# Performance work log

Hardware: AMD Instinct MI355X
Metric: run time of the kernel (lower is better)

The kernel has to match this reference:

```python
import jax, jax.numpy as jnp
import numpy as np

B, S, D_MODEL = 2, 1024, 1024
N_HEADS, D_QK, D_V = 16, 64, 64
MAX_ROPE, MAX_REL = 2048, 128
ATTN_SCALE = 8.0  # sqrt(d_qk)
BASE = 10000.0


def _rope_table():
    # sinusoidal buffer from RoPE.__init__ (pos_type='sinusoidal')
    pos = np.arange(MAX_ROPE).reshape(-1, 1)
    ang = pos / np.power(BASE, np.arange(0, D_QK, 2).reshape(1, -1) / D_QK)
    W = np.zeros((MAX_ROPE, D_QK), dtype=np.float32)
    W[:, 0::2] = np.sin(ang)
    W[:, 1::2] = np.cos(ang)
    return jnp.asarray(W)


def _apply_rope(x, pe):
    # x: [b,n,s,d], pe: [b,s,d]
    cos = jnp.tile(pe[:, :, 1::2], (1, 1, 2))[:, None, :, :]  # [b,1,s,d]
    sin = jnp.tile(pe[:, :, 0::2], (1, 1, 2))[:, None, :, :]
    half = D_QK // 2
    x2 = jnp.concatenate([-x[..., half:], x[..., :half]], axis=-1)
    return x * cos + x2 * sin


def setup_inputs() -> dict:
    key = jax.random.key(0)
    ks = jax.random.split(key, 12)
    w_scale = 1.0 / np.sqrt(D_MODEL)
    inp = {
        'query': jax.random.normal(ks[0], (B, S, D_MODEL), jnp.float32),
        'key': jax.random.normal(ks[1], (B, S, D_MODEL), jnp.float32),
        'value': jax.random.normal(ks[2], (B, S, D_MODEL), jnp.float32),
        'attn_mask': jnp.broadcast_to(jnp.triu(jnp.ones((S, S), bool), 1), (B, S, S)),
        'q_pos_ids': jnp.broadcast_to(jnp.arange(S, dtype=jnp.int32), (B, S)),
        'kv_pos_ids': jnp.broadcast_to(jnp.arange(S, dtype=jnp.int32), (B, S)),
        'W_q': jax.random.normal(ks[3], (N_HEADS * D_QK, D_MODEL), jnp.float32) * w_scale,
        'b_q': jnp.zeros((N_HEADS * D_QK,), jnp.float32),
        'W_k': jax.random.normal(ks[4], (N_HEADS * D_QK, D_MODEL), jnp.float32) * w_scale,
        'b_k': jnp.zeros((N_HEADS * D_QK,), jnp.float32),
        'W_v': jax.random.normal(ks[5], (N_HEADS * D_V, D_MODEL), jnp.float32) * w_scale,
        'b_v': jnp.zeros((N_HEADS * D_V,), jnp.float32),
        'W_o': jax.random.normal(ks[6], (D_MODEL, N_HEADS * D_V), jnp.float32) * w_scale,
        'b_o': jnp.zeros((D_MODEL,), jnp.float32),
        'rel_k_table': jax.random.normal(ks[7], (2 * MAX_REL + 1, D_QK), jnp.float32) * 0.02,
        'rel_v_table': jax.random.normal(ks[8], (2 * MAX_REL + 1, D_V), jnp.float32) * 0.02,
        'w_pre': jax.random.normal(ks[9], (N_HEADS, N_HEADS), jnp.float32) * (1.0 / np.sqrt(N_HEADS)),
        'w_post': jax.random.normal(ks[10], (N_HEADS, N_HEADS), jnp.float32) * (1.0 / np.sqrt(N_HEADS)),
    }
    return inp


def reference(query, key, value, attn_mask, q_pos_ids, kv_pos_ids,
              W_q, b_q, W_k, b_k, W_v, b_v, W_o, b_o,
              rel_k_table, rel_v_table, w_pre, w_post):
    # projections: F.linear(x, W) = x @ W.T, then + bias
    q = (query @ W_q.T + b_q).reshape(B, S, N_HEADS, D_QK).transpose(0, 2, 1, 3)
    k = (key @ W_k.T + b_k).reshape(B, S, N_HEADS, D_QK).transpose(0, 2, 1, 3)
    v = (value @ W_v.T + b_v).reshape(B, S, N_HEADS, D_V).transpose(0, 2, 1, 3)

    # RoPE (sinusoidal buffer, no grad)
    rope_W = _rope_table()
    q = _apply_rope(q, rope_W[q_pos_ids])
    k = _apply_rope(k, rope_W[kv_pos_ids])

    # relative position embeddings (learned tables)
    rel_dis = q_pos_ids[:, :, None] - kv_pos_ids[:, None, :]        # [b,q,k]
    idx = jnp.clip(rel_dis, -MAX_REL, MAX_REL) + MAX_REL
    pos_key = rel_k_table[idx]                                       # [b,q,k,d_qk]
    pos_value = rel_v_table[idx]                                     # [b,q,k,d_v]

    scores = jnp.einsum('bnqd,bnkd->bnqk', q, k)
    scores = scores + jnp.einsum('bnqd,bqkd->bnqk', q, pos_key)
    scores = scores / ATTN_SCALE
    scores = jnp.einsum('bnqk,nm->bmqk', scores, w_pre)              # talking heads pre-softmax
    scores = jnp.where(attn_mask[:, None, :, :], -10000.0, scores)
    attn = jax.nn.softmax(scores, axis=-1)
    attn = jnp.einsum('bmqk,mn->bnqk', attn, w_post)                 # talking heads post-softmax

    out = jnp.einsum('bnqk,bnkd->bnqd', attn, v)
    out = out + jnp.einsum('bnqk,bqkd->bnqd', attn, pos_value)

    out = out.transpose(0, 2, 1, 3).reshape(B, S, N_HEADS * D_V)
    out = out @ W_o.T + b_o
    return out
```

## Files before the change

kernel.cpp:

```cpp
#include <hip/hip_runtime.h>

#define SEQ 1024

typedef short v8s __attribute__((ext_vector_type(8)));
typedef float v4f __attribute__((ext_vector_type(4)));

__device__ __forceinline__ short f2bfs(float f){
  unsigned int u = __float_as_uint(f);
  u += 0x7fffu + ((u >> 16) & 1u);
  return (short)(u >> 16);
}
__device__ __forceinline__ float bfl(short s){
  return __uint_as_float(((unsigned int)(unsigned short)s) << 16);
}

__global__ __launch_bounds__(256) void conv_kernel(
    const float* __restrict__ q, const float* __restrict__ k, const float* __restrict__ v,
    const float* __restrict__ wq, const float* __restrict__ wk2, const float* __restrict__ wv2,
    const float* __restrict__ wo, unsigned short* __restrict__ dst)
{
  size_t e0 = ((size_t)blockIdx.x * 256 + threadIdx.x) * 8;
  const float* src; size_t off;
  if      (e0 <  2097152){ src = q;   off = e0; }
  else if (e0 <  4194304){ src = k;   off = e0 - 2097152; }
  else if (e0 <  6291456){ src = v;   off = e0 - 4194304; }
  else if (e0 <  7340032){ src = wq;  off = e0 - 6291456; }
  else if (e0 <  8388608){ src = wk2; off = e0 - 7340032; }
  else if (e0 <  9437184){ src = wv2; off = e0 - 8388608; }
  else                   { src = wo;  off = e0 - 9437184; }
  float4 a = *(const float4*)(src + off);
  float4 b = *(const float4*)(src + off + 4);
  v8s o = { f2bfs(a.x), f2bfs(a.y), f2bfs(a.z), f2bfs(a.w),
            f2bfs(b.x), f2bfs(b.y), f2bfs(b.z), f2bfs(b.w) };
  *(v8s*)(dst + e0) = o;
}

__device__ __forceinline__ void gemm_body(
    const unsigned short* __restrict__ A16,
    const unsigned short* __restrict__ P1, const unsigned short* __restrict__ P2,
    const unsigned short* __restrict__ P3,
    const unsigned short* __restrict__ W16,
    const float* __restrict__ bias, void* __restrict__ outv,
    const int* __restrict__ pos_ids, int mode)
{
  __shared__ short As[2][64][40];
  __shared__ short Ws[2][128][40];

  int t = threadIdx.x;
  int lane = t & 63, wave = t >> 6;
  int l15 = lane & 15, quad = lane >> 4;
  int wm = wave >> 1, wn = wave & 1;
  int row0 = blockIdx.y << 6;
  int col0 = blockIdx.x << 7;

  v4f acc[4];
  #pragma unroll
  for (int j = 0; j < 4; j++) acc[j] = (v4f){0.f, 0.f, 0.f, 0.f};

  int ar = t >> 2, ac = (t & 3) * 8;
  int wr = t >> 2, wc = (t & 3) * 8;
  size_t abase = (size_t)(row0 + ar)*1024 + ac;
  size_t wbase = (size_t)(col0 + wr)*1024 + wc;

  if (t < 256){
    if (P1){
      v8s x0 = *(const v8s*)(A16 + abase);
      v8s x1 = *(const v8s*)(P1 + abase);
      v8s x2 = *(const v8s*)(P2 + abase);
      v8s x3 = *(const v8s*)(P3 + abase);
      v8s o;
      #pragma unroll
      for (int jj = 0; jj < 8; jj++)
        o[jj] = f2bfs(bfl(x0[jj]) + bfl(x1[jj]) + bfl(x2[jj]) + bfl(x3[jj]));
      *(v8s*)&As[0][ar][ac] = o;
    } else {
      *(v8s*)&As[0][ar][ac] = *(const v8s*)(A16 + abase);
    }
  }
  *(v8s*)&Ws[0][wr][wc] = *(const v8s*)(W16 + wbase);
  __syncthreads();

  int cur = 0;
  for (int kt = 0; kt < 1024; kt += 32){
    bool nxt = (kt + 32) < 1024;
    v8s a_st, x1s, x2s, x3s, w_st;
    if (nxt){
      if (t < 256){
        a_st = *(const v8s*)(A16 + abase + kt + 32);
        if (P1){
          x1s = *(const v8s*)(P1 + abase + kt + 32);
          x2s = *(const v8s*)(P2 + abase + kt + 32);
          x3s = *(const v8s*)(P3 + abase + kt + 32);
        }
      }
      w_st = *(const v8s*)(W16 + wbase + kt + 32);
    }

    v8s af = *(v8s*)&As[cur][wm*16 + l15][quad*8];
    v8s bfq[4];
    #pragma unroll
    for (int j = 0; j < 4; j++) bfq[j] = *(v8s*)&Ws[cur][wn*64 + j*16 + l15][quad*8];
    #pragma unroll
    for (int j = 0; j < 4; j++)
      acc[j] = __builtin_amdgcn_mfma_f32_16x16x32_bf16(af, bfq[j], acc[j], 0, 0, 0);

    if (nxt){
      if (t < 256){
        if (P1){
          v8s o;
          #pragma unroll
          for (int jj = 0; jj < 8; jj++)
            o[jj] = f2bfs(bfl(a_st[jj]) + bfl(x1s[jj]) + bfl(x2s[jj]) + bfl(x3s[jj]));
          *(v8s*)&As[cur ^ 1][ar][ac] = o;
        } else {
          *(v8s*)&As[cur ^ 1][ar][ac] = a_st;
        }
      }
      *(v8s*)&Ws[cur ^ 1][wr][wc] = w_st;
      __syncthreads();
      cur ^= 1;
    }
  }

  int rbase = row0 + wm*16 + quad*4;
  if (mode == 1){
    unsigned short* o16 = (unsigned short*)outv;
    int pos[4];
    #pragma unroll
    for (int r = 0; r < 4; r++){
      int p = pos_ids[rbase + r];
      pos[r] = p < 0 ? 0 : (p > 2047 ? 2047 : p);
    }
    float fr0 = exp2f(-0.4152410118609203f * (float)l15);
    float fr1 = exp2f(-0.4152410118609203f * (float)(16 + l15));
    float csv[2][4], snv[2][4];
    #pragma unroll
    for (int r = 0; r < 4; r++){
      float a0 = (float)pos[r] * fr0;
      float a1 = (float)pos[r] * fr1;
      csv[0][r] = __cosf(a0); snv[0][r] = __sinf(a0);
      csv[1][r] = __cosf(a1); snv[1][r] = __sinf(a1);
    }
    #pragma unroll
    for (int j = 0; j < 4; j++){
      int gcol = col0 + wn*64 + j*16 + l15;
      float bs = bias[gcol];
      float bp = bias[gcol ^ 32];
      #pragma unroll
      for (int r = 0; r < 4; r++){
        float x = acc[j][r] + bs;
        float p = acc[j ^ 2][r] + bp;
        float cs = csv[j & 1][r];
        float sn = snv[j & 1][r];
        float o = (j < 2) ? (x*cs - p*sn) : (x*cs + p*sn);
        o16[(size_t)(rbase + r)*1024 + gcol] = (unsigned short)f2bfs(o);
      }
    }
  } else if (mode == 2){
    unsigned short* o16 = (unsigned short*)outv;
    int bb = rbase >> 10, s0 = rbase & 1023;
    #pragma unroll
    for (int j = 0; j < 4; j++){
      int gcol = col0 + wn*64 + j*16 + l15;
      float bs = bias[gcol];
      unsigned int w0 = ((unsigned int)(unsigned short)f2bfs(acc[j][0] + bs)) |
                        (((unsigned int)(unsigned short)f2bfs(acc[j][1] + bs)) << 16);
      unsigned int w1 = ((unsigned int)(unsigned short)f2bfs(acc[j][2] + bs)) |
                        (((unsigned int)(unsigned short)f2bfs(acc[j][3] + bs)) << 16);
      uint2 pk; pk.x = w0; pk.y = w1;
      *(uint2*)&o16[((size_t)(bb*1024 + gcol))*1024 + s0] = pk;
    }
  } else {
    float* o32 = (float*)outv;
    #pragma unroll
    for (int j = 0; j < 4; j++){
      int gcol = col0 + wn*64 + j*16 + l15;
      float bs = bias[gcol];
      #pragma unroll
      for (int r = 0; r < 4; r++)
        o32[(size_t)(rbase + r)*1024 + gcol] = acc[j][r] + bs;
    }
  }
}

__global__ __launch_bounds__(512) void gemm_qkv_kernel(
    const unsigned short* __restrict__ qa, const unsigned short* __restrict__ ka,
    const unsigned short* __restrict__ va,
    const unsigned short* __restrict__ wq, const unsigned short* __restrict__ wk,
    const unsigned short* __restrict__ wv,
    const float* __restrict__ bq, const float* __restrict__ bk, const float* __restrict__ bv,
    unsigned short* __restrict__ oq, unsigned short* __restrict__ ok, unsigned short* __restrict__ ov,
    const int* __restrict__ qpos, const int* __restrict__ kpos)
{
  int z = blockIdx.z;
  const unsigned short* A16 = (z == 0) ? qa : (z == 1) ? ka : va;
  const unsigned short* W16 = (z == 0) ? wq : (z == 1) ? wk : wv;
  const float* bias         = (z == 0) ? bq : (z == 1) ? bk : bv;
  unsigned short* outp      = (z == 0) ? oq : (z == 1) ? ok : ov;
  const int* pos            = (z == 1) ? kpos : qpos;
  int mode                  = (z == 2) ? 2 : 1;
  gemm_body(A16, nullptr, nullptr, nullptr, W16, bias, (void*)outp, pos, mode);
}

__global__ __launch_bounds__(512) void gemm_o_kernel(
    const unsigned short* __restrict__ c0, const unsigned short* __restrict__ c1,
    const unsigned short* __restrict__ c2, const unsigned short* __restrict__ c3,
    const unsigned short* __restrict__ wo, const float* __restrict__ bo,
    float* __restrict__ outp)
{
  gemm_body(c0, c1, c2, c3, wo, bo, (void*)outp, nullptr, 0);
}

__global__ __launch_bounds__(1024) void attn_pass1(
    const unsigned short* __restrict__ qw, const unsigned short* __restrict__ kw,
    const float* __restrict__ relk, const float* __restrict__ wpre_g,
    unsigned short* __restrict__ Sp, float* __restrict__ Lp)
{
  __shared__ short U_t[2][512][20];
  __shared__ short W_l[16][16][48];
  __shared__ short relk_s[129][68];

  int t = threadIdx.x;
  int h = t >> 6, lane = t & 63;
  int l15 = lane & 15, quad = lane >> 4;
  int bid = blockIdx.x;
  int quarter = bid & 3;
  int b = (bid >> 2) & 1;
  int qt = 63 - (bid >> 3);
  int q0 = qt << 4;
  int nkt = (qt + 2) >> 1;
  int hq = qt >> 1;
  int offt = hq*(hq+1) + ((qt & 1) ? (hq + 1) : 0);
  unsigned short* Sbase = Sp + ((size_t)(b*1056 + offt)) * 8192;

  for (int e = t; e < 129*64; e += 1024)
    relk_s[e >> 6][e & 63] = f2bfs(relk[(size_t)(128 + (e >> 6))*64 + (e & 63)]);

  v8s awp;
  #pragma unroll
  for (int jj = 0; jj < 8; jj++){
    int n = quad*8 + jj;
    awp[jj] = (n < 16) ? f2bfs(wpre_g[n*16 + l15]) : (short)0;
  }
  v8s aq[2];
  {
    const unsigned short* qb = qw + ((size_t)(b*SEQ + q0 + l15))*1024 + h*64;
    #pragma unroll
    for (int c = 0; c < 2; c++) aq[c] = *(const v8s*)(qb + c*32 + quad*8);
  }
  __syncthreads();

  v4f cinf = (v4f){0.f,0.f,0.f,0.f};
  #pragma unroll
  for (int c = 0; c < 2; c++){
    v8s binf = *(v8s*)&relk_s[128][c*32 + quad*8];
    cinf = __builtin_amdgcn_mfma_f32_16x16x32_bf16(aq[c], binf, cinf, 0, 0, 0);
  }

  float l_part[4] = {0.f, 0.f, 0.f, 0.f};

  v8s kc[2][2];
  if (quarter < nkt){
    int k0 = quarter << 5;
    #pragma unroll
    for (int ct = 0; ct < 2; ct++){
      const unsigned short* kb = kw + ((size_t)(b*SEQ + k0 + ct*16 + l15))*1024 + h*64;
      #pragma unroll
      for (int c = 0; c < 2; c++) kc[ct][c] = *(const v8s*)(kb + c*32 + quad*8);
    }
  }

  int buf = 0;
  for (int ci = quarter; ci < nkt; ci += 4){
    int k0 = ci << 5;
    int r_lo = q0 - k0 - 31;
    bool far = (r_lo >= 128);

    v4f cqk[2];
    #pragma unroll
    for (int ct = 0; ct < 2; ct++){
      v4f acc = (v4f){0.f,0.f,0.f,0.f};
      #pragma unroll
      for (int c = 0; c < 2; c++)
        acc = __builtin_amdgcn_mfma_f32_16x16x32_bf16(aq[c], kc[ct][c], acc, 0, 0, 0);
      cqk[ct] = acc;
    }
    {
      int cin = ci + 4;
      int k0n = ((cin < nkt) ? cin : ci) << 5;
      #pragma unroll
      for (int ct = 0; ct < 2; ct++){
        const unsigned short* kb = kw + ((size_t)(b*SEQ + k0n + ct*16 + l15))*1024 + h*64;
        #pragma unroll
        for (int c = 0; c < 2; c++) kc[ct][c] = *(const v8s*)(kb + c*32 + quad*8);
      }
    }

    if (!far){
      #pragma unroll
      for (int pt = 0; pt < 3; pt++){
        int rr = r_lo + pt*16 + l15; rr = rr < 0 ? 0 : (rr > 128 ? 128 : rr);
        v4f acc = (v4f){0.f,0.f,0.f,0.f};
        #pragma unroll
        for (int c = 0; c < 2; c++){
          v8s rv = *(v8s*)&relk_s[rr][c*32 + quad*8];
          acc = __builtin_amdgcn_mfma_f32_16x16x32_bf16(aq[c], rv, acc, 0, 0, 0);
        }
        #pragma unroll
        for (int reg = 0; reg < 4; reg++)
          W_l[h][quad*4 + reg][pt*16 + l15] = f2bfs(acc[reg]);
      }
    }
    #pragma unroll
    for (int ct = 0; ct < 2; ct++)
      #pragma unroll
      for (int reg = 0; reg < 4; reg++){
        int i = quad*4 + reg, j = ct*16 + l15;
        float wv = far ? cinf[reg] : bfl(W_l[h][i][i - j + 31]);
        U_t[buf][i*32 + j][h] = f2bfs((cqk[ct][reg] + wv) * 0.125f);
      }
    __syncthreads();

    v4f cs[2];
    #pragma unroll
    for (int ct = 0; ct < 2; ct++){
      v8s bu = (v8s){0,0,0,0,0,0,0,0};
      if (quad < 2) bu = *(v8s*)&U_t[buf][h*32 + ct*16 + l15][quad*8];
      cs[ct] = __builtin_amdgcn_mfma_f32_16x16x32_bf16(awp, bu, (v4f){0.f,0.f,0.f,0.f}, 0, 0, 0);
    }
    unsigned short* stile = Sbase + (size_t)ci * 8192;
    #pragma unroll
    for (int ct = 0; ct < 2; ct++){
      bool vv = (k0 + ct*16 + l15) <= (q0 + h);
      short pb16[4];
      #pragma unroll
      for (int reg = 0; reg < 4; reg++){
        float p = vv ? __expf(cs[ct][reg]) : 0.f;
        l_part[reg] += p;
        pb16[reg] = f2bfs(p);
      }
      uint2 pk;
      pk.x = ((unsigned int)(unsigned short)pb16[0]) | (((unsigned int)(unsigned short)pb16[1]) << 16);
      pk.y = ((unsigned int)(unsigned short)pb16[2]) | (((unsigned int)(unsigned short)pb16[3]) << 16);
      *(uint2*)(stile + ((size_t)((h*2 + ct)*64 + quad*16 + l15))*4) = pk;
    }
    buf ^= 1;
  }

  #pragma unroll
  for (int reg = 0; reg < 4; reg++){
    float sm = l_part[reg];
    sm += __shfl_xor(sm, 1, 64);
    sm += __shfl_xor(sm, 2, 64);
    sm += __shfl_xor(sm, 4, 64);
    sm += __shfl_xor(sm, 8, 64);
    l_part[reg] = sm;
  }
  size_t pb = ((((size_t)b*64 + qt)*4 + quarter)*16 + h)*16;
  if (l15 == 0){
    #pragma unroll
    for (int reg = 0; reg < 4; reg++)
      Lp[pb + quad*4 + reg] = l_part[reg];
  }
}

__global__ __launch_bounds__(1024) void attn_pass2(
    const unsigned short* __restrict__ Sp, const unsigned short* __restrict__ vwT,
    const float* __restrict__ relv, const float* __restrict__ wpost_g,
    const float* __restrict__ Lp,
    unsigned short* __restrict__ c0, unsigned short* __restrict__ c1,
    unsigned short* __restrict__ c2, unsigned short* __restrict__ c3)
{
  __shared__ short U_t[512][20];
  __shared__ short Pp[2][16][16][40];
  __shared__ short relv_s[129][66];
  __shared__ float il_f[16][17], Srow[16][17];

  int t = threadIdx.x;
  int h = t >> 6, lane = t & 63;
  int l15 = lane & 15, quad = lane >> 4;
  int bid = blockIdx.x;
  int quarter = bid & 3;
  int b = (bid >> 2) & 1;
  int qt = 63 - (bid >> 3);
  int q0 = qt << 4;
  int nkt = (qt + 2) >> 1;
  int hq = qt >> 1;
  int offt = hq*(hq+1) + ((qt & 1) ? (hq + 1) : 0);
  const unsigned short* Sbase = Sp + ((size_t)(b*1056 + offt)) * 8192;
  unsigned short* ctx = (quarter == 0) ? c0 : (quarter == 1) ? c1 : (quarter == 2) ? c2 : c3;

  for (int e = t; e < 129*64; e += 1024)
    relv_s[e >> 6][e & 63] = f2bfs(relv[(size_t)(128 + (e >> 6))*64 + (e & 63)]);
  if (t < 256){
    int i = t >> 4, n = t & 15;
    size_t b0 = ((((size_t)b*64 + qt)*4 + 0)*16 + i)*16 + n;
    float l = 0.f;
    #pragma unroll
    for (int qd = 0; qd < 4; qd++) l += Lp[b0 + qd*256];
    il_f[i][n] = 1.f / l;
  }
  v8s awq;
  #pragma unroll
  for (int jj = 0; jj < 8; jj++){
    int n = quad*8 + jj;
    awq[jj] = (n < 16) ? f2bfs(wpost_g[n*16 + l15]) : (short)0;
  }
  __syncthreads();

  v4f o_acc[4];
  #pragma unroll
  for (int dt = 0; dt < 4; dt++) o_acc[dt] = (v4f){0.f,0.f,0.f,0.f};
  float sr_part[4] = {0.f, 0.f, 0.f, 0.f};

  const unsigned short* vtb = vwT + ((size_t)(b*1024 + h*64))*1024;

  uint4 sv;
  v8s bvc[4];
  if (quarter < nkt){
    sv = *(const uint4*)(Sbase + (size_t)quarter*8192 + (size_t)t*8);
    int k0 = quarter << 5;
    #pragma unroll
    for (int dt = 0; dt < 4; dt++)
      bvc[dt] = *(const v8s*)(vtb + (size_t)(dt*16 + l15)*1024 + k0 + quad*8);
  }

  int pbuf = 0;
  for (int ci = quarter; ci < nkt; ci += 4){
    int k0 = ci << 5;
    int r_lo = q0 - k0 - 31;
    bool far = (r_lo >= 128);

    #pragma unroll
    for (int g = 0; g < 2; g++){
      unsigned int w0 = (g == 0) ? sv.x : sv.z;
      unsigned int w1 = (g == 0) ? sv.y : sv.w;
      int v = t*2 + g;
      int i = v >> 7, ct = (v >> 6) & 1, quadv = (v >> 4) & 3, lv = v & 15;
      int j = ct*16 + lv;
      short at[4];
      unsigned short ss[4] = { (unsigned short)(w0 & 0xffff), (unsigned short)(w0 >> 16),
                               (unsigned short)(w1 & 0xffff), (unsigned short)(w1 >> 16) };
      #pragma unroll
      for (int reg = 0; reg < 4; reg++){
        int n = quadv*4 + reg;
        at[reg] = f2bfs(bfl((short)ss[reg]) * il_f[i][n]);
      }
      unsigned int lo = ((unsigned int)(unsigned short)at[0]) | (((unsigned int)(unsigned short)at[1]) << 16);
      unsigned int hi = ((unsigned int)(unsigned short)at[2]) | (((unsigned int)(unsigned short)at[3]) << 16);
      uint2 pk; pk.x = lo; pk.y = hi;
      *(uint2*)&U_t[i*32 + j][quadv*4] = pk;
    }

    v4f cp[2];
    #pragma unroll
    for (int ct = 0; ct < 2; ct++){
      v8s bu = (v8s){0,0,0,0,0,0,0,0};
      if (quad < 2) bu = *(v8s*)&U_t[h*32 + ct*16 + l15][quad*8];
      cp[ct] = __builtin_amdgcn_mfma_f32_16x16x32_bf16(awq, bu, (v4f){0.f,0.f,0.f,0.f}, 0, 0, 0);
    }
    #pragma unroll
    for (int ct = 0; ct < 2; ct++)
      #pragma unroll
      for (int reg = 0; reg < 4; reg++){
        int n = quad*4 + reg, j = ct*16 + l15;
        Pp[pbuf][n][h][j] = f2bfs(cp[ct][reg]);
      }
    if (far){
      #pragma unroll
      for (int reg = 0; reg < 4; reg++)
        sr_part[reg] += cp[0][reg] + cp[1][reg];
    }
    __syncthreads();

    {
      int cin = ci + 4;
      int cld = (cin < nkt) ? cin : ci;
      sv = *(const uint4*)(Sbase + (size_t)cld*8192 + (size_t)t*8);
    }

    v8s ap = *(v8s*)&Pp[pbuf][h][l15][quad*8];
    #pragma unroll
    for (int dt = 0; dt < 4; dt++)
      o_acc[dt] = __builtin_amdgcn_mfma_f32_16x16x32_bf16(ap, bvc[dt], o_acc[dt], 0, 0, 0);
    {
      int cin = ci + 4;
      int k0n = ((cin < nkt) ? cin : ci) << 5;
      #pragma unroll
      for (int dt = 0; dt < 4; dt++)
        bvc[dt] = *(const v8s*)(vtb + (size_t)(dt*16 + l15)*1024 + k0n + quad*8);
    }
    if (!far){
      #pragma unroll
      for (int ch = 0; ch < 2; ch++){
        v8s at2;
        #pragma unroll
        for (int jj = 0; jj < 8; jj++){
          int jx = l15 + 31 - (ch*32 + quad*8 + jj);
          at2[jj] = ((unsigned)jx < 32u) ? Pp[pbuf][h][l15][jx] : (short)0;
        }
        #pragma unroll
        for (int dt = 0; dt < 4; dt++){
          v8s br;
          #pragma unroll
          for (int jj = 0; jj < 8; jj++){
            int rr = r_lo + ch*32 + quad*8 + jj;
            rr = rr < 0 ? 0 : (rr > 128 ? 128 : rr);
            br[jj] = relv_s[rr][dt*16 + l15];
          }
          o_acc[dt] = __builtin_amdgcn_mfma_f32_16x16x32_bf16(at2, br, o_acc[dt], 0, 0, 0);
        }
      }
    }
    pbuf ^= 1;
  }

  #pragma unroll
  for (int reg = 0; reg < 4; reg++){
    float s = sr_part[reg];
    s += __shfl_xor(s, 1, 64);
    s += __shfl_xor(s, 2, 64);
    s += __shfl_xor(s, 4, 64);
    s += __shfl_xor(s, 8, 64);
    if (l15 == 0) Srow[quad*4 + reg][h] = s;
  }
  __syncthreads();

  #pragma unroll
  for (int dt = 0; dt < 4; dt++)
    #pragma unroll
    for (int reg = 0; reg < 4; reg++){
      float o = o_acc[dt][reg] + Srow[h][quad*4 + reg] * bfl(relv_s[128][dt*16 + l15]);
      ctx[((size_t)(b*SEQ + q0 + quad*4 + reg))*1024 + h*64 + dt*16 + l15] = (unsigned short)f2bfs(o);
    }
}

extern "C" void kernel_launch(void* const* d_in, const int* in_sizes, int n_in,
                              void* d_out, int out_size, void* d_ws, size_t ws_size,
                              hipStream_t stream)
{
  int ip = -1;
  for (int i = 0; i < n_in; i++){
    if (in_sizes[i] == 2048){ ip = i; break; }
  }
  if (ip < 0) ip = 4;

  const float* query = (const float*)d_in[0];
  const float* key   = (const float*)d_in[1];
  const float* value = (const float*)d_in[2];
  const int* qpos = (const int*)d_in[ip];
  const int* kpos = (const int*)d_in[ip + 1];
  const float* Wq    = (const float*)d_in[ip + 2];
  const float* bq    = (const float*)d_in[ip + 3];
  const float* Wk    = (const float*)d_in[ip + 4];
  const float* bk    = (const float*)d_in[ip + 5];
  const float* Wv    = (const float*)d_in[ip + 6];
  const float* b_v   = (const float*)d_in[ip + 7];
  const float* Wo    = (const float*)d_in[ip + 8];
  const float* bo    = (const float*)d_in[ip + 9];
  const float* relk  = (const float*)d_in[ip + 10];
  const float* relv  = (const float*)d_in[ip + 11];
  const float* wpre  = (const float*)d_in[ip + 12];
  const float* wpost = (const float*)d_in[ip + 13];

  char* ws = (char*)d_ws;
  unsigned short* conv  = (unsigned short*)(ws + 524288);
  unsigned short* qbf   = conv;
  unsigned short* kbf   = conv + 2097152;
  unsigned short* vbf   = conv + 4194304;
  unsigned short* wqbf  = conv + 6291456;
  unsigned short* wkbf  = conv + 7340032;
  unsigned short* wvbf  = conv + 8388608;
  unsigned short* wobf  = conv + 9437184;
  unsigned short* q_ws  = (unsigned short*)(ws + 21495808);
  unsigned short* k_ws  = (unsigned short*)(ws + 25690112);
  unsigned short* v_ws  = (unsigned short*)(ws + 29884416);
  unsigned short* ctx0  = (unsigned short*)(ws + 34078720);
  unsigned short* ctx1  = (unsigned short*)(ws + 38273024);
  unsigned short* ctx2  = (unsigned short*)(ws + 42467328);
  unsigned short* ctx3  = (unsigned short*)(ws + 46661632);
  unsigned short* Sp    = (unsigned short*)(ws + 50855936);
  float* Lp             = (float*)(ws + 85983232);

  hipLaunchKernelGGL(conv_kernel, dim3(5120), dim3(256), 0, stream,
                     query, key, value, Wq, Wk, Wv, Wo, conv);
  hipLaunchKernelGGL(gemm_qkv_kernel, dim3(8, 32, 3), dim3(512), 0, stream,
                     qbf, kbf, vbf, wqbf, wkbf, wvbf, bq, bk, b_v,
                     q_ws, k_ws, v_ws, qpos, kpos);
  hipLaunchKernelGGL(attn_pass1, dim3(512), dim3(1024), 0, stream,
                     q_ws, k_ws, relk, wpre, Sp, Lp);
  hipLaunchKernelGGL(attn_pass2, dim3(512), dim3(1024), 0, stream,
                     Sp, v_ws, relv, wpost, Lp, ctx0, ctx1, ctx2, ctx3);
  hipLaunchKernelGGL(gemm_o_kernel, dim3(8, 32), dim3(512), 0, stream,
                     ctx0, ctx1, ctx2, ctx3, wobf, bo, (float*)d_out);
}
```

Measured before the change: 248.9 us.

## Store score tiles in MFMA operand layout and fold 1/l into post weights

Result: no change. 249.9 us (+0.4%).

```diff
diff --git a/kernel.cpp b/kernel.cpp
--- a/kernel.cpp
+++ b/kernel.cpp
@@ -342,7 +342,7 @@
       uint2 pk;
       pk.x = ((unsigned int)(unsigned short)pb16[0]) | (((unsigned int)(unsigned short)pb16[1]) << 16);
       pk.y = ((unsigned int)(unsigned short)pb16[2]) | (((unsigned int)(unsigned short)pb16[3]) << 16);
-      *(uint2*)(stile + ((size_t)((h*2 + ct)*64 + quad*16 + l15))*4) = pk;
+      *(uint2*)(stile + (size_t)(h*32 + ct*16 + l15)*16 + quad*4) = pk;
     }
     buf ^= 1;
   }
@@ -371,7 +371,6 @@
     unsigned short* __restrict__ c0, unsigned short* __restrict__ c1,
     unsigned short* __restrict__ c2, unsigned short* __restrict__ c3)
 {
-  __shared__ short U_t[512][20];
   __shared__ short Pp[2][16][16][40];
   __shared__ short relv_s[129][66];
   __shared__ float il_f[16][17], Srow[16][17];
@@ -400,13 +399,16 @@
     for (int qd = 0; qd < 4; qd++) l += Lp[b0 + qd*256];
     il_f[i][n] = 1.f / l;
   }
-  v8s awq;
-  #pragma unroll
-  for (int jj = 0; jj < 8; jj++){
-    int n = quad*8 + jj;
-    awq[jj] = (n < 16) ? f2bfs(wpost_g[n*16 + l15]) : (short)0;
-  }
   __syncthreads();
+
+  v8s awq = (v8s){0,0,0,0,0,0,0,0};
+  if (quad < 2){
+    #pragma unroll
+    for (int jj = 0; jj < 8; jj++){
+      int m = quad*8 + jj;
+      awq[jj] = f2bfs(wpost_g[m*16 + l15] * il_f[h][m]);
+    }
+  }
 
   v4f o_acc[4];
   #pragma unroll
@@ -415,10 +417,15 @@
 
   const unsigned short* vtb = vwT + ((size_t)(b*1024 + h*64))*1024;
 
-  uint4 sv;
+  v8s spc[2];
   v8s bvc[4];
   if (quarter < nkt){
-    sv = *(const uint4*)(Sbase + (size_t)quarter*8192 + (size_t)t*8);
+    const unsigned short* st = Sbase + (size_t)quarter*8192;
+    if (quad < 2){
+      #pragma unroll
+      for (int ct = 0; ct < 2; ct++)
+        spc[ct] = *(const v8s*)(st + (size_t)(h*32 + ct*16 + l15)*16 + quad*8);
+    }
     int k0 = quarter << 5;
     #pragma unroll
     for (int dt = 0; dt < 4; dt++)
@@ -431,32 +438,11 @@
     int r_lo = q0 - k0 - 31;
     bool far = (r_lo >= 128);
 
-    #pragma unroll
-    for (int g = 0; g < 2; g++){
-      unsigned int w0 = (g == 0) ? sv.x : sv.z;
-      unsigned int w1 = (g == 0) ? sv.y : sv.w;
-      int v = t*2 + g;
-      int i = v >> 7, ct = (v >> 6) & 1, quadv = (v >> 4) & 3, lv = v & 15;
-      int j = ct*16 + lv;
-      short at[4];
-      unsigned short ss[4] = { (unsigned short)(w0 & 0xffff), (unsigned short)(w0 >> 16),
-                               (unsigned short)(w1 & 0xffff), (unsigned short)(w1 >> 16) };
-      #pragma unroll
-      for (int reg = 0; reg < 4; reg++){
-        int n = quadv*4 + reg;
-        at[reg] = f2bfs(bfl((short)ss[reg]) * il_f[i][n]);
-      }
-      unsigned int lo = ((unsigned int)(unsigned short)at[0]) | (((unsigned int)(unsigned short)at[1]) << 16);
-      unsigned int hi = ((unsigned int)(unsigned short)at[2]) | (((unsigned int)(unsigned short)at[3]) << 16);
-      uint2 pk; pk.x = lo; pk.y = hi;
-      *(uint2*)&U_t[i*32 + j][quadv*4] = pk;
-    }
-
     v4f cp[2];
     #pragma unroll
     for (int ct = 0; ct < 2; ct++){
       v8s bu = (v8s){0,0,0,0,0,0,0,0};
-      if (quad < 2) bu = *(v8s*)&U_t[h*32 + ct*16 + l15][quad*8];
+      if (quad < 2) bu = spc[ct];
       cp[ct] = __builtin_amdgcn_mfma_f32_16x16x32_bf16(awq, bu, (v4f){0.f,0.f,0.f,0.f}, 0, 0, 0);
     }
     #pragma unroll
@@ -476,7 +462,12 @@
     {
       int cin = ci + 4;
       int cld = (cin < nkt) ? cin : ci;
-      sv = *(const uint4*)(Sbase + (size_t)cld*8192 + (size_t)t*8);
+      const unsigned short* st = Sbase + (size_t)cld*8192;
+      if (quad < 2){
+        #pragma unroll
+        for (int ct = 0; ct < 2; ct++)
+          spc[ct] = *(const v8s*)(st + (size_t)(h*32 + ct*16 + l15)*16 + quad*8);
+      }
     }
 
     v8s ap = *(v8s*)&Pp[pbuf][h][l15][quad*8];
```
